# Kernel optimization log

Hardware: AMD Instinct MI355X
Metric: run time of the kernel (lower is better)

## Reference

```python
import jax, jax.numpy as jnp
import numpy as np

B, S, D, H = 4, 2048, 512, 8
DK = D // H


def setup_inputs() -> dict:
    key = jax.random.key(0)
    ks = jax.random.split(key, 11)
    scale = 1.0 / np.sqrt(D)
    inp = {
        'q': jax.random.normal(ks[0], (B, S, D), jnp.float32),
        'k': jax.random.normal(ks[1], (B, S, D), jnp.float32),
        'v': jax.random.normal(ks[2], (B, S, D), jnp.float32),
        'mask': jnp.tril(jnp.ones((S, S), jnp.int32))[None, None, :, :],  # [1,1,S,S] causal
        'w_q': jax.random.normal(ks[3], (D, D), jnp.float32) * scale,
        'b_q': jnp.zeros((D,), jnp.float32),
        'w_k': jax.random.normal(ks[4], (D, D), jnp.float32) * scale,
        'b_k': jnp.zeros((D,), jnp.float32),
        'w_v': jax.random.normal(ks[5], (D, D), jnp.float32) * scale,
        'b_v': jnp.zeros((D,), jnp.float32),
        'w_o': jax.random.normal(ks[6], (D, D), jnp.float32) * scale,
        'b_o': jnp.zeros((D,), jnp.float32),
    }
    return inp


def reference(q, k, v, mask, w_q, b_q, w_k, b_k, w_v, b_v, w_o, b_o):
    # QKV projections (nn.Linear: x @ W^T + b)
    def split_heads(x):  # [B,S,D] -> [B,H,S,DK]
        return x.reshape(B, S, H, DK).transpose(0, 2, 1, 3)

    qh = split_heads(q @ w_q.T + b_q)
    kh = split_heads(k @ w_k.T + b_k)
    vh = split_heads(v @ w_v.T + b_v)

    scores = jnp.einsum('bhqd,bhkd->bhqk', qh, kh) / jnp.sqrt(jnp.float32(DK))
    scores = jnp.where(mask == 0, jnp.float32(-1e9), scores)
    attn = jax.nn.softmax(scores, axis=-1)  # dropout is identity in eval
    ctx = jnp.einsum('bhqk,bhkd->bhqd', attn, vh)  # [B,H,S,DK]
    ctx = ctx.transpose(0, 2, 1, 3).reshape(B, S, D)
    return ctx @ w_o.T + b_o
```

## Files before the change

### kernel.cpp

```cpp
#include <hip/hip_runtime.h>
#include <hip/hip_bf16.h>


#define BATCH  4
#define SLEN   2048
#define DMODEL 512
#define NHEAD  8
#define DHEAD  64
#define MROWS  (BATCH * SLEN)

#define NQ ((size_t)MROWS * DMODEL)
#define NW ((size_t)DMODEL * DMODEL)
#define NB ((size_t)DMODEL)
#define CVT_TOTAL (3 * NQ + 4 * NW + 4 * NB)

#define SCALE_L2E 0.180336880f

typedef short bf16x8 __attribute__((ext_vector_type(8)));
typedef float f32x4  __attribute__((ext_vector_type(4)));

typedef unsigned int __attribute__((address_space(1))) glb_u32_t;
typedef unsigned int __attribute__((address_space(3))) lds_u32_t;

__device__ __forceinline__ void async_copy16(const unsigned short* g, unsigned short* l) {
    __builtin_amdgcn_global_load_lds((glb_u32_t*)g, (lds_u32_t*)l, 16, 0, 0);
}

__device__ __forceinline__ float bf2f(unsigned short u) {
    union { unsigned int i; float f; } v; v.i = ((unsigned int)u) << 16; return v.f;
}
__device__ __forceinline__ unsigned short f2bf(float f) {
    union { float f; unsigned int i; } v; v.f = f;
    unsigned int x = v.i;
    return (unsigned short)((x + 0x7fffu + ((x >> 16) & 1u)) >> 16);
}
__device__ __forceinline__ unsigned int pkbf(float a, float b) {
    union { __hip_bfloat162 h; unsigned int u; } cv;
    cv.h = __float22bfloat162_rn(float2{a, b});
    return cv.u;
}

__device__ __forceinline__ void wait0_barrier() {
    asm volatile("s_waitcnt vmcnt(0)" ::: "memory");
    __builtin_amdgcn_s_barrier();
    asm volatile("" ::: "memory");
}

__global__ __launch_bounds__(256)
void cvt_kernel(const float* __restrict__ q, const float* __restrict__ k,
                const float* __restrict__ v,
                const float* __restrict__ wq, const float* __restrict__ wk,
                const float* __restrict__ wv, const float* __restrict__ wo,
                const float* __restrict__ bq, const float* __restrict__ bk,
                const float* __restrict__ bv, const float* __restrict__ bo,
                unsigned short* __restrict__ dst)
{
    const size_t i4 = ((size_t)blockIdx.x * 256 + threadIdx.x) * 4;
    if (i4 >= CVT_TOTAL) return;
    const float* src;
    size_t off;
    if      (i4 <     NQ)          { src = q;  off = i4; }
    else if (i4 < 2 * NQ)          { src = k;  off = i4 - NQ; }
    else if (i4 < 3 * NQ)          { src = v;  off = i4 - 2 * NQ; }
    else if (i4 < 3 * NQ + NW)     { src = wq; off = i4 - 3 * NQ; }
    else if (i4 < 3 * NQ + 2 * NW) { src = wk; off = i4 - 3 * NQ - NW; }
    else if (i4 < 3 * NQ + 3 * NW) { src = wv; off = i4 - 3 * NQ - 2 * NW; }
    else if (i4 < 3 * NQ + 4 * NW) { src = wo; off = i4 - 3 * NQ - 3 * NW; }
    else if (i4 < 3 * NQ + 4 * NW + NB)     { src = bq; off = i4 - 3 * NQ - 4 * NW; }
    else if (i4 < 3 * NQ + 4 * NW + 2 * NB) { src = bk; off = i4 - 3 * NQ - 4 * NW - NB; }
    else if (i4 < 3 * NQ + 4 * NW + 3 * NB) { src = bv; off = i4 - 3 * NQ - 4 * NW - 2 * NB; }
    else                                    { src = bo; off = i4 - 3 * NQ - 4 * NW - 3 * NB; }
    const float4 f = *(const float4*)(src + off);
    ushort4 o;
    o.x = f2bf(f.x); o.y = f2bf(f.y); o.z = f2bf(f.z); o.w = f2bf(f.w);
    *(ushort4*)(dst + i4) = o;
}

template <typename OutT>
__device__ __forceinline__ void gemm_body(const unsigned short* __restrict__ A,
                                          const unsigned short* __restrict__ W,
                                          const unsigned short* __restrict__ bias,
                                          OutT* __restrict__ C, int mode)
{
    __shared__ __align__(16) unsigned short As[2][128 * 32];
    __shared__ __align__(16) unsigned short Bs[2][128 * 32];

    const int tid  = threadIdx.x;
    const int wave = tid >> 6;
    const int lane = tid & 63;
    const int l15  = lane & 15;
    const int quad = lane >> 4;
    const int m0   = blockIdx.x * 128;
    const int n0   = blockIdx.y * 128;
    const int wm   = (wave & 1) * 64;
    const int wn   = (wave >> 1) * 64;
    const int srow = lane >> 2;
    const int scol = (((lane & 3) ^ (srow & 3)) * 8);
    const int rsw  = (quad ^ (l15 & 3)) * 8;

    auto stage = [&](int k0, int buf) {
        async_copy16(A + (size_t)(m0 + wave * 16 + srow) * DMODEL + k0 + scol, As[buf] + wave * 512);
        async_copy16(A + (size_t)(m0 + (wave + 4) * 16 + srow) * DMODEL + k0 + scol, As[buf] + (wave + 4) * 512);
        async_copy16(W + (size_t)(n0 + wave * 16 + srow) * DMODEL + k0 + scol, Bs[buf] + wave * 512);
        async_copy16(W + (size_t)(n0 + (wave + 4) * 16 + srow) * DMODEL + k0 + scol, Bs[buf] + (wave + 4) * 512);
    };

    f32x4 acc[4][4] = {};
    stage(0, 0);

    #pragma unroll 1
    for (int kt = 0; kt < 16; kt++) {
        const int cur = kt & 1;
        wait0_barrier();
        if (kt < 15) stage((kt + 1) * 32, cur ^ 1);

        bf16x8 af[4], bfr[4];
        #pragma unroll
        for (int i = 0; i < 4; i++)
            af[i] = *(const bf16x8*)(As[cur] + (wm + i * 16 + l15) * 32 + rsw);
        #pragma unroll
        for (int j = 0; j < 4; j++)
            bfr[j] = *(const bf16x8*)(Bs[cur] + (wn + j * 16 + l15) * 32 + rsw);
        #pragma unroll
        for (int i = 0; i < 4; i++)
            #pragma unroll
            for (int j = 0; j < 4; j++)
                acc[i][j] = __builtin_amdgcn_mfma_f32_16x16x32_bf16(af[i], bfr[j], acc[i][j], 0, 0, 0);
    }

    if (mode == 2) {
        #pragma unroll
        for (int j = 0; j < 4; j++) {
            const int col = n0 + wn + j * 16 + l15;
            const float bv = bf2f(bias[col]);
            const int hh = col >> 6, dk = col & 63;
            #pragma unroll
            for (int i = 0; i < 4; i++) {
                const int row = m0 + wm + i * 16 + quad * 4;
                const int bb = row >> 11, s = row & 2047;
                uint2 o2;
                o2.x = pkbf(acc[i][j][0] + bv, acc[i][j][1] + bv);
                o2.y = pkbf(acc[i][j][2] + bv, acc[i][j][3] + bv);
                *(uint2*)((unsigned short*)C + ((size_t)((bb * NHEAD + hh) * DHEAD + dk)) * SLEN + s) = o2;
            }
        }
    } else {
        const float oscale = (mode == 0) ? SCALE_L2E : 1.0f;
        #pragma unroll
        for (int j = 0; j < 4; j++) {
            const int col = n0 + wn + j * 16 + l15;
            const float bv = bf2f(bias[col]);
            #pragma unroll
            for (int i = 0; i < 4; i++) {
                const int row = m0 + wm + i * 16 + quad * 4;
                #pragma unroll
                for (int r = 0; r < 4; r++) {
                    const float val = (acc[i][j][r] + bv) * oscale;
                    if constexpr (sizeof(OutT) == 4)
                        C[(size_t)(row + r) * DMODEL + col] = val;
                    else
                        C[(size_t)(row + r) * DMODEL + col] = f2bf(val);
                }
            }
        }
    }
}

__global__ __launch_bounds__(256, 3)
void qkv_gemm_kernel(const unsigned short* __restrict__ qin,
                     const unsigned short* __restrict__ kin,
                     const unsigned short* __restrict__ vin,
                     const unsigned short* __restrict__ wq,
                     const unsigned short* __restrict__ bq,
                     const unsigned short* __restrict__ wk,
                     const unsigned short* __restrict__ bk,
                     const unsigned short* __restrict__ wv,
                     const unsigned short* __restrict__ bv,
                     unsigned short* __restrict__ qh,
                     unsigned short* __restrict__ kh,
                     unsigned short* __restrict__ vt)
{
    const int z = blockIdx.z;
    const unsigned short* A    = (z == 0) ? qin : (z == 1) ? kin : vin;
    const unsigned short* W    = (z == 0) ? wq  : (z == 1) ? wk  : wv;
    const unsigned short* bias = (z == 0) ? bq  : (z == 1) ? bk  : bv;
    unsigned short*       C    = (z == 0) ? qh  : (z == 1) ? kh  : vt;
    gemm_body<unsigned short>(A, W, bias, C, z);
}

__global__ __launch_bounds__(256, 3)
void oproj_gemm_kernel(const unsigned short* __restrict__ ctx,
                       const unsigned short* __restrict__ wo,
                       const unsigned short* __restrict__ bo,
                       float* __restrict__ out)
{
    gemm_body<float>(ctx, wo, bo, out, 3);
}

__global__ __launch_bounds__(256, 4)
void attn_kernel(const unsigned short* __restrict__ qh,
                 const unsigned short* __restrict__ kh,
                 const unsigned short* __restrict__ vt,
                 unsigned short* __restrict__ ctx)
{
    __shared__ __align__(16) unsigned short Ks[2][64 * 64];
    __shared__ __align__(16) unsigned short Vs[2][64 * 64];
    __shared__ __align__(16) unsigned short Ps[4 * 16 * 64];

    const int tid  = threadIdx.x;
    const int wave = tid >> 6;
    const int lane = tid & 63;
    const int l15  = lane & 15;
    const int quad = lane >> 4;

    const int bh = blockIdx.x;
    const int x  = blockIdx.y;
    const int g  = x & 7, s = x >> 3;
    const int qt = (s == 0) ? g : (s == 1) ? 15 - g : (s == 2) ? 16 + g : 31 - g;
    const int b  = bh >> 3;
    const int h  = bh & 7;

    const size_t base = (size_t)b * SLEN * DMODEL + (size_t)h * DHEAD;
    const unsigned short* Q  = qh + base;
    const unsigned short* K  = kh + base;
    const unsigned short* VT = vt + (size_t)bh * DHEAD * SLEN;

    const int krow_l = lane >> 3;
    const int kcol_l = ((lane & 7) ^ (krow_l & 7)) * 8;

    const int qrow = qt * 64 + wave * 16 + l15;
    bf16x8 qf0 = *(const bf16x8*)(Q + (size_t)qrow * DMODEL + quad * 8);
    bf16x8 qf1 = *(const bf16x8*)(Q + (size_t)qrow * DMODEL + 32 + quad * 8);

    f32x4 oacc[4] = {};
    float lsum = 0.0f;

    unsigned short* Pw = Ps + wave * (16 * 64);
    const int ktiles = qt + 1;

    auto stageKV = [&](int kt, int buf) {
        async_copy16(K + (size_t)(kt * 64 + wave * 8 + krow_l) * DMODEL + kcol_l,
                     Ks[buf] + wave * 512);
        async_copy16(K + (size_t)(kt * 64 + (wave + 4) * 8 + krow_l) * DMODEL + kcol_l,
                     Ks[buf] + (wave + 4) * 512);
        async_copy16(VT + (size_t)(wave * 8 + krow_l) * SLEN + kt * 64 + kcol_l,
                     Vs[buf] + wave * 512);
        async_copy16(VT + (size_t)((wave + 4) * 8 + krow_l) * SLEN + kt * 64 + kcol_l,
                     Vs[buf] + (wave + 4) * 512);
    };

    stageKV(0, 0);

    #pragma unroll 1
    for (int kt = 0; kt < ktiles; kt++) {
        const int cur = kt & 1;
        wait0_barrier();
        if (kt + 1 < ktiles) stageKV(kt + 1, cur ^ 1);

        f32x4 sacc[4] = {};
        #pragma unroll
        for (int kk = 0; kk < 2; kk++) {
            const bf16x8 qf = kk ? qf1 : qf0;
            #pragma unroll
            for (int j = 0; j < 4; j++) {
                bf16x8 kf = *(const bf16x8*)(Ks[cur] + (j * 16 + l15) * 64
                                                + (((kk * 4 + quad) ^ (l15 & 7)) * 8));
                sacc[j] = __builtin_amdgcn_mfma_f32_16x16x32_bf16(kf, qf, sacc[j], 0, 0, 0);
            }
        }

        if (kt == qt) {
            #pragma unroll
            for (int j = 0; j < 4; j++)
                #pragma unroll
                for (int r = 0; r < 4; r++) {
                    const int kv = kt * 64 + j * 16 + quad * 4 + r;
                    if (kv > qrow) sacc[j][r] = -1e30f;
                }
        }

        #pragma unroll
        for (int j = 0; j < 4; j++) {
            const float p0 = exp2f(sacc[j][0]);
            const float p1 = exp2f(sacc[j][1]);
            const float p2v = exp2f(sacc[j][2]);
            const float p3 = exp2f(sacc[j][3]);
            lsum += (p0 + p1) + (p2v + p3);
            uint2 pw;
            pw.x = pkbf(p0, p1);
            pw.y = pkbf(p2v, p3);
            const int chunk = (j * 2 + (quad >> 1)) ^ (l15 & 7);
            *(uint2*)(Pw + l15 * 64 + chunk * 8 + (quad & 1) * 4) = pw;
        }
        asm volatile("s_waitcnt lgkmcnt(0)" ::: "memory");

        #pragma unroll
        for (int kk = 0; kk < 2; kk++) {
            bf16x8 pf = *(const bf16x8*)(Pw + l15 * 64 + (((kk * 4 + quad) ^ (l15 & 7)) * 8));
            #pragma unroll
            for (int jd = 0; jd < 4; jd++) {
                bf16x8 vf = *(const bf16x8*)(Vs[cur] + (jd * 16 + l15) * 64
                                                + (((kk * 4 + quad) ^ (l15 & 7)) * 8));
                oacc[jd] = __builtin_amdgcn_mfma_f32_16x16x32_bf16(vf, pf, oacc[jd], 0, 0, 0);
            }
        }
    }

    lsum += __shfl_xor(lsum, 16, 64);
    lsum += __shfl_xor(lsum, 32, 64);
    const float invl = 1.0f / lsum;

    #pragma unroll
    for (int jd = 0; jd < 4; jd++) {
        uint2 o2;
        o2.x = pkbf(oacc[jd][0] * invl, oacc[jd][1] * invl);
        o2.y = pkbf(oacc[jd][2] * invl, oacc[jd][3] * invl);
        *(uint2*)(ctx + base + (size_t)qrow * DMODEL + jd * 16 + quad * 4) = o2;
    }
}

extern "C" void kernel_launch(void* const* d_in, const int* in_sizes, int n_in,
                              void* d_out, int out_size, void* d_ws, size_t ws_size,
                              hipStream_t stream)
{
    const float* q   = (const float*)d_in[0];
    const float* k   = (const float*)d_in[1];
    const float* v   = (const float*)d_in[2];
    const float* w_q = (const float*)d_in[4];
    const float* b_q = (const float*)d_in[5];
    const float* w_k = (const float*)d_in[6];
    const float* b_k = (const float*)d_in[7];
    const float* w_v = (const float*)d_in[8];
    const float* b_v = (const float*)d_in[9];
    const float* w_o = (const float*)d_in[10];
    const float* b_o = (const float*)d_in[11];
    float* out = (float*)d_out;

    unsigned short* ws = (unsigned short*)d_ws;
    unsigned short* qb  = ws;
    unsigned short* kb  = ws + NQ;
    unsigned short* vb  = ws + 2 * NQ;
    unsigned short* wqb = ws + 3 * NQ;
    unsigned short* wkb = wqb + NW;
    unsigned short* wvb = wkb + NW;
    unsigned short* wob = wvb + NW;
    unsigned short* bqb = wob + NW;
    unsigned short* bkb = bqb + NB;
    unsigned short* bvb = bkb + NB;
    unsigned short* bob = bvb + NB;
    unsigned short* qh  = bob + NB;
    unsigned short* kh  = qh + NQ;
    unsigned short* vt  = kh + NQ;
    unsigned short* ctx = vt + NQ;

    dim3 blk(256);
    hipLaunchKernelGGL(cvt_kernel, dim3((unsigned)(CVT_TOTAL / 4 / 256)), blk, 0, stream,
                       q, k, v, w_q, w_k, w_v, w_o, b_q, b_k, b_v, b_o, ws);
    hipLaunchKernelGGL(qkv_gemm_kernel, dim3(MROWS / 128, DMODEL / 128, 3), blk, 0, stream,
                       qb, kb, vb, wqb, bqb, wkb, bkb, wvb, bvb, qh, kh, vt);
    hipLaunchKernelGGL(attn_kernel, dim3(BATCH * NHEAD, 32), blk, 0, stream,
                       qh, kh, vt, ctx);
    hipLaunchKernelGGL(oproj_gemm_kernel, dim3(MROWS / 128, DMODEL / 128), blk, 0, stream,
                       ctx, wob, bob, out);
}
```

Before: 198.1 us.

## Pair complementary causal query tiles per block to share K/V staging

Each attention block now processes two query tiles, g and 31-g, in a single pass over key tiles. For the first g+1 key tiles both tiles' scores and PV products come from the same staged K/V in LDS, so K/V loads and barriers for those tiles are shared. Every block also gets the same total amount of causal work, which balances the load. The grid is halved, the P scratch buffer doubled and launch bounds relaxed to 2 to allow more registers, at the cost of fewer resident waves to hide latency.

New measurement: 198.7 us. Within noise of the previous version (+0.3%).

```diff
diff --git a/kernel.cpp b/kernel.cpp
--- a/kernel.cpp
+++ b/kernel.cpp
@@ -197,7 +197,7 @@
     gemm_body<float>(ctx, wo, bo, out, 3);
 }
 
-__global__ __launch_bounds__(256, 4)
+__global__ __launch_bounds__(256, 2)
 void attn_kernel(const unsigned short* __restrict__ qh,
                  const unsigned short* __restrict__ kh,
                  const unsigned short* __restrict__ vt,
@@ -205,7 +205,7 @@
 {
     __shared__ __align__(16) unsigned short Ks[2][64 * 64];
     __shared__ __align__(16) unsigned short Vs[2][64 * 64];
-    __shared__ __align__(16) unsigned short Ps[4 * 16 * 64];
+    __shared__ __align__(16) unsigned short Ps[4 * 2 * 16 * 64];
 
     const int tid  = threadIdx.x;
     const int wave = tid >> 6;
@@ -215,8 +215,9 @@
 
     const int bh = blockIdx.x;
     const int x  = blockIdx.y;
-    const int g  = x & 7, s = x >> 3;
-    const int qt = (s == 0) ? g : (s == 1) ? 15 - g : (s == 2) ? 16 + g : 31 - g;
+    const int g  = (x < 8) ? x : 23 - x;
+    const int qta = g;
+    const int qtb = 31 - g;
     const int b  = bh >> 3;
     const int h  = bh & 7;
 
@@ -228,15 +229,19 @@
     const int krow_l = lane >> 3;
     const int kcol_l = ((lane & 7) ^ (krow_l & 7)) * 8;
 
-    const int qrow = qt * 64 + wave * 16 + l15;
-    bf16x8 qf0 = *(const bf16x8*)(Q + (size_t)qrow * DMODEL + quad * 8);
-    bf16x8 qf1 = *(const bf16x8*)(Q + (size_t)qrow * DMODEL + 32 + quad * 8);
-
-    f32x4 oacc[4] = {};
-    float lsum = 0.0f;
-
-    unsigned short* Pw = Ps + wave * (16 * 64);
-    const int ktiles = qt + 1;
+    const int qrow_a = qta * 64 + wave * 16 + l15;
+    const int qrow_b = qtb * 64 + wave * 16 + l15;
+    const bf16x8 qa0 = *(const bf16x8*)(Q + (size_t)qrow_a * DMODEL + quad * 8);
+    const bf16x8 qa1 = *(const bf16x8*)(Q + (size_t)qrow_a * DMODEL + 32 + quad * 8);
+    const bf16x8 qb0 = *(const bf16x8*)(Q + (size_t)qrow_b * DMODEL + quad * 8);
+    const bf16x8 qb1 = *(const bf16x8*)(Q + (size_t)qrow_b * DMODEL + 32 + quad * 8);
+
+    f32x4 oacc_a[4] = {};
+    f32x4 oacc_b[4] = {};
+    float lsum_a = 0.0f, lsum_b = 0.0f;
+
+    unsigned short* Pa = Ps + (wave * 2 + 0) * (16 * 64);
+    unsigned short* Pb = Ps + (wave * 2 + 1) * (16 * 64);
 
     auto stageKV = [&](int kt, int buf) {
         async_copy16(K + (size_t)(kt * 64 + wave * 8 + krow_l) * DMODEL + kcol_l,
@@ -249,36 +254,7 @@
                      Vs[buf] + (wave + 4) * 512);
     };
 
-    stageKV(0, 0);
-
-    #pragma unroll 1
-    for (int kt = 0; kt < ktiles; kt++) {
-        const int cur = kt & 1;
-        wait0_barrier();
-        if (kt + 1 < ktiles) stageKV(kt + 1, cur ^ 1);
-
-        f32x4 sacc[4] = {};
-        #pragma unroll
-        for (int kk = 0; kk < 2; kk++) {
-            const bf16x8 qf = kk ? qf1 : qf0;
-            #pragma unroll
-            for (int j = 0; j < 4; j++) {
-                bf16x8 kf = *(const bf16x8*)(Ks[cur] + (j * 16 + l15) * 64
-                                                + (((kk * 4 + quad) ^ (l15 & 7)) * 8));
-                sacc[j] = __builtin_amdgcn_mfma_f32_16x16x32_bf16(kf, qf, sacc[j], 0, 0, 0);
-            }
-        }
-
-        if (kt == qt) {
-            #pragma unroll
-            for (int j = 0; j < 4; j++)
-                #pragma unroll
-                for (int r = 0; r < 4; r++) {
-                    const int kv = kt * 64 + j * 16 + quad * 4 + r;
-                    if (kv > qrow) sacc[j][r] = -1e30f;
-                }
-        }
-
+    auto softmax_pack = [&](f32x4* sacc, unsigned short* Pw, float& lsum) {
         #pragma unroll
         for (int j = 0; j < 4; j++) {
             const float p0 = exp2f(sacc[j][0]);
@@ -292,30 +268,112 @@
             const int chunk = (j * 2 + (quad >> 1)) ^ (l15 & 7);
             *(uint2*)(Pw + l15 * 64 + chunk * 8 + (quad & 1) * 4) = pw;
         }
-        asm volatile("s_waitcnt lgkmcnt(0)" ::: "memory");
-
-        #pragma unroll
-        for (int kk = 0; kk < 2; kk++) {
-            bf16x8 pf = *(const bf16x8*)(Pw + l15 * 64 + (((kk * 4 + quad) ^ (l15 & 7)) * 8));
-            #pragma unroll
-            for (int jd = 0; jd < 4; jd++) {
-                bf16x8 vf = *(const bf16x8*)(Vs[cur] + (jd * 16 + l15) * 64
-                                                + (((kk * 4 + quad) ^ (l15 & 7)) * 8));
-                oacc[jd] = __builtin_amdgcn_mfma_f32_16x16x32_bf16(vf, pf, oacc[jd], 0, 0, 0);
+    };
+
+    auto diag_mask = [&](f32x4* sacc, int kt, int qrow) {
+        #pragma unroll
+        for (int j = 0; j < 4; j++)
+            #pragma unroll
+            for (int r = 0; r < 4; r++) {
+                const int kv = kt * 64 + j * 16 + quad * 4 + r;
+                if (kv > qrow) sacc[j][r] = -1e30f;
+            }
+    };
+
+    const int nkt = 32 - g;
+    stageKV(0, 0);
+
+    #pragma unroll 1
+    for (int kt = 0; kt < nkt; kt++) {
+        const int cur = kt & 1;
+        wait0_barrier();
+        if (kt + 1 < nkt) stageKV(kt + 1, cur ^ 1);
+
+        if (kt <= g) {
+            f32x4 sa[4] = {}, sb[4] = {};
+            #pragma unroll
+            for (int kk = 0; kk < 2; kk++) {
+                const bf16x8 qfa = kk ? qa1 : qa0;
+                const bf16x8 qfb = kk ? qb1 : qb0;
+                #pragma unroll
+                for (int j = 0; j < 4; j++) {
+                    bf16x8 kf = *(const bf16x8*)(Ks[cur] + (j * 16 + l15) * 64
+                                                    + (((kk * 4 + quad) ^ (l15 & 7)) * 8));
+                    sb[j] = __builtin_amdgcn_mfma_f32_16x16x32_bf16(kf, qfb, sb[j], 0, 0, 0);
+                    sa[j] = __builtin_amdgcn_mfma_f32_16x16x32_bf16(kf, qfa, sa[j], 0, 0, 0);
+                }
+            }
+            if (kt == qta) diag_mask(sa, kt, qrow_a);
+            softmax_pack(sa, Pa, lsum_a);
+            softmax_pack(sb, Pb, lsum_b);
+            asm volatile("s_waitcnt lgkmcnt(0)" ::: "memory");
+
+            #pragma unroll
+            for (int kk = 0; kk < 2; kk++) {
+                bf16x8 pfa = *(const bf16x8*)(Pa + l15 * 64 + (((kk * 4 + quad) ^ (l15 & 7)) * 8));
+                bf16x8 pfb = *(const bf16x8*)(Pb + l15 * 64 + (((kk * 4 + quad) ^ (l15 & 7)) * 8));
+                #pragma unroll
+                for (int jd = 0; jd < 4; jd++) {
+                    bf16x8 vf = *(const bf16x8*)(Vs[cur] + (jd * 16 + l15) * 64
+                                                    + (((kk * 4 + quad) ^ (l15 & 7)) * 8));
+                    oacc_a[jd] = __builtin_amdgcn_mfma_f32_16x16x32_bf16(vf, pfa, oacc_a[jd], 0, 0, 0);
+                    oacc_b[jd] = __builtin_amdgcn_mfma_f32_16x16x32_bf16(vf, pfb, oacc_b[jd], 0, 0, 0);
+                }
+            }
+        } else {
+            f32x4 sb[4] = {};
+            #pragma unroll
+            for (int kk = 0; kk < 2; kk++) {
+                const bf16x8 qfb = kk ? qb1 : qb0;
+                #pragma unroll
+                for (int j = 0; j < 4; j++) {
+                    bf16x8 kf = *(const bf16x8*)(Ks[cur] + (j * 16 + l15) * 64
+                                                    + (((kk * 4 + quad) ^ (l15 & 7)) * 8));
+                    sb[j] = __builtin_amdgcn_mfma_f32_16x16x32_bf16(kf, qfb, sb[j], 0, 0, 0);
+                }
+            }
+            if (kt == qtb) diag_mask(sb, kt, qrow_b);
+            softmax_pack(sb, Pb, lsum_b);
+            asm volatile("s_waitcnt lgkmcnt(0)" ::: "memory");
+
+            #pragma unroll
+            for (int kk = 0; kk < 2; kk++) {
+                bf16x8 pfb = *(const bf16x8*)(Pb + l15 * 64 + (((kk * 4 + quad) ^ (l15 & 7)) * 8));
+                #pragma unroll
+                for (int jd = 0; jd < 4; jd++) {
+                    bf16x8 vf = *(const bf16x8*)(Vs[cur] + (jd * 16 + l15) * 64
+                                                    + (((kk * 4 + quad) ^ (l15 & 7)) * 8));
+                    oacc_b[jd] = __builtin_amdgcn_mfma_f32_16x16x32_bf16(vf, pfb, oacc_b[jd], 0, 0, 0);
+                }
             }
         }
     }
 
-    lsum += __shfl_xor(lsum, 16, 64);
-    lsum += __shfl_xor(lsum, 32, 64);
-    const float invl = 1.0f / lsum;
-
-    #pragma unroll
-    for (int jd = 0; jd < 4; jd++) {
-        uint2 o2;
-        o2.x = pkbf(oacc[jd][0] * invl, oacc[jd][1] * invl);
-        o2.y = pkbf(oacc[jd][2] * invl, oacc[jd][3] * invl);
-        *(uint2*)(ctx + base + (size_t)qrow * DMODEL + jd * 16 + quad * 4) = o2;
+    {
+        float la = lsum_a;
+        la += __shfl_xor(la, 16, 64);
+        la += __shfl_xor(la, 32, 64);
+        const float invla = 1.0f / la;
+        #pragma unroll
+        for (int jd = 0; jd < 4; jd++) {
+            uint2 o2;
+            o2.x = pkbf(oacc_a[jd][0] * invla, oacc_a[jd][1] * invla);
+            o2.y = pkbf(oacc_a[jd][2] * invla, oacc_a[jd][3] * invla);
+            *(uint2*)(ctx + base + (size_t)qrow_a * DMODEL + jd * 16 + quad * 4) = o2;
+        }
+    }
+    {
+        float lb = lsum_b;
+        lb += __shfl_xor(lb, 16, 64);
+        lb += __shfl_xor(lb, 32, 64);
+        const float invlb = 1.0f / lb;
+        #pragma unroll
+        for (int jd = 0; jd < 4; jd++) {
+            uint2 o2;
+            o2.x = pkbf(oacc_b[jd][0] * invlb, oacc_b[jd][1] * invlb);
+            o2.y = pkbf(oacc_b[jd][2] * invlb, oacc_b[jd][3] * invlb);
+            *(uint2*)(ctx + base + (size_t)qrow_b * DMODEL + jd * 16 + quad * 4) = o2;
+        }
     }
 }
 
@@ -358,7 +416,7 @@
                        q, k, v, w_q, w_k, w_v, w_o, b_q, b_k, b_v, b_o, ws);
     hipLaunchKernelGGL(qkv_gemm_kernel, dim3(MROWS / 128, DMODEL / 128, 3), blk, 0, stream,
                        qb, kb, vb, wqb, bqb, wkb, bkb, wvb, bvb, qh, kh, vt);
-    hipLaunchKernelGGL(attn_kernel, dim3(BATCH * NHEAD, 32), blk, 0, stream,
+    hipLaunchKernelGGL(attn_kernel, dim3(BATCH * NHEAD, 16), blk, 0, stream,
                        qh, kh, vt, ctx);
     hipLaunchKernelGGL(oproj_gemm_kernel, dim3(MROWS / 128, DMODEL / 128), blk, 0, stream,
                        ctx, wob, bob, out);
```

## Fuse pipeline into one cooperative persistent kernel with grid barriers

Applied to the files above, without the earlier changes.

Replaces the four launches with a single cooperative kernel of 768 blocks that converts the weights, runs the QKV projection, attention and output projection, and separates the stages with global atomic barriers. The QKV GEMM now loads the fp32 activations directly into LDS and converts them to bf16 in registers, so the separate pass that wrote bf16 copies of q, k and v is gone. Attention tiles are paired long with short to balance causal work across blocks, and the output projection moves to 64x64 tiles so the grid is covered. The intent is to cut launch overhead and the activation conversion traffic. In exchange it adds spin-barrier costs, a memset, and a fallback multi-kernel path if the cooperative launch fails.

New measurement: 696.3 us. +251.5%, slower.

```diff
diff --git a/kernel.cpp b/kernel.cpp
--- a/kernel.cpp
+++ b/kernel.cpp
@@ -12,7 +12,9 @@
 #define NQ ((size_t)MROWS * DMODEL)
 #define NW ((size_t)DMODEL * DMODEL)
 #define NB ((size_t)DMODEL)
-#define CVT_TOTAL (3 * NQ + 4 * NW + 4 * NB)
+#define CVTW_TOTAL (4 * NW + 4 * NB)
+
+#define GRID_P 768
 
 #define SCALE_L2E 0.180336880f
 
@@ -22,7 +24,7 @@
 typedef unsigned int __attribute__((address_space(1))) glb_u32_t;
 typedef unsigned int __attribute__((address_space(3))) lds_u32_t;
 
-__device__ __forceinline__ void async_copy16(const unsigned short* g, unsigned short* l) {
+__device__ __forceinline__ void async16(const void* g, void* l) {
     __builtin_amdgcn_global_load_lds((glb_u32_t*)g, (lds_u32_t*)l, 16, 0, 0);
 }
 
@@ -46,81 +48,80 @@
     asm volatile("" ::: "memory");
 }
 
-__global__ __launch_bounds__(256)
-void cvt_kernel(const float* __restrict__ q, const float* __restrict__ k,
-                const float* __restrict__ v,
-                const float* __restrict__ wq, const float* __restrict__ wk,
-                const float* __restrict__ wv, const float* __restrict__ wo,
-                const float* __restrict__ bq, const float* __restrict__ bk,
-                const float* __restrict__ bv, const float* __restrict__ bo,
-                unsigned short* __restrict__ dst)
-{
-    const size_t i4 = ((size_t)blockIdx.x * 256 + threadIdx.x) * 4;
-    if (i4 >= CVT_TOTAL) return;
-    const float* src;
-    size_t off;
-    if      (i4 <     NQ)          { src = q;  off = i4; }
-    else if (i4 < 2 * NQ)          { src = k;  off = i4 - NQ; }
-    else if (i4 < 3 * NQ)          { src = v;  off = i4 - 2 * NQ; }
-    else if (i4 < 3 * NQ + NW)     { src = wq; off = i4 - 3 * NQ; }
-    else if (i4 < 3 * NQ + 2 * NW) { src = wk; off = i4 - 3 * NQ - NW; }
-    else if (i4 < 3 * NQ + 3 * NW) { src = wv; off = i4 - 3 * NQ - 2 * NW; }
-    else if (i4 < 3 * NQ + 4 * NW) { src = wo; off = i4 - 3 * NQ - 3 * NW; }
-    else if (i4 < 3 * NQ + 4 * NW + NB)     { src = bq; off = i4 - 3 * NQ - 4 * NW; }
-    else if (i4 < 3 * NQ + 4 * NW + 2 * NB) { src = bk; off = i4 - 3 * NQ - 4 * NW - NB; }
-    else if (i4 < 3 * NQ + 4 * NW + 3 * NB) { src = bv; off = i4 - 3 * NQ - 4 * NW - 2 * NB; }
-    else                                    { src = bo; off = i4 - 3 * NQ - 4 * NW - 3 * NB; }
-    const float4 f = *(const float4*)(src + off);
-    ushort4 o;
-    o.x = f2bf(f.x); o.y = f2bf(f.y); o.z = f2bf(f.z); o.w = f2bf(f.w);
-    *(ushort4*)(dst + i4) = o;
-}
-
-template <typename OutT>
-__device__ __forceinline__ void gemm_body(const unsigned short* __restrict__ A,
-                                          const unsigned short* __restrict__ W,
-                                          const unsigned short* __restrict__ bias,
-                                          OutT* __restrict__ C, int mode)
-{
-    __shared__ __align__(16) unsigned short As[2][128 * 32];
-    __shared__ __align__(16) unsigned short Bs[2][128 * 32];
+__device__ __forceinline__ void gbar(unsigned* c) {
+    __syncthreads();
+    if (threadIdx.x == 0) {
+        __threadfence();
+        __hip_atomic_fetch_add(c, 1u, __ATOMIC_RELEASE, __HIP_MEMORY_SCOPE_AGENT);
+        while (__hip_atomic_load(c, __ATOMIC_ACQUIRE, __HIP_MEMORY_SCOPE_AGENT) < gridDim.x)
+            __builtin_amdgcn_s_sleep(8);
+    }
+    __syncthreads();
+}
+
+__device__ __forceinline__ void qkv_body(const float* __restrict__ A,
+                                         const unsigned short* __restrict__ W,
+                                         const unsigned short* __restrict__ bias,
+                                         unsigned short* __restrict__ C,
+                                         int mode, int m0, int n0,
+                                         unsigned char* smem)
+{
+    float*          Asf = (float*)smem;
+    unsigned short* Bs  = (unsigned short*)(smem + 32768);
 
     const int tid  = threadIdx.x;
     const int wave = tid >> 6;
     const int lane = tid & 63;
     const int l15  = lane & 15;
     const int quad = lane >> 4;
-    const int m0   = blockIdx.x * 128;
-    const int n0   = blockIdx.y * 128;
     const int wm   = (wave & 1) * 64;
     const int wn   = (wave >> 1) * 64;
     const int srow = lane >> 2;
     const int scol = (((lane & 3) ^ (srow & 3)) * 8);
-    const int rsw  = (quad ^ (l15 & 3)) * 8;
-
-    auto stage = [&](int k0, int buf) {
-        async_copy16(A + (size_t)(m0 + wave * 16 + srow) * DMODEL + k0 + scol, As[buf] + wave * 512);
-        async_copy16(A + (size_t)(m0 + (wave + 4) * 16 + srow) * DMODEL + k0 + scol, As[buf] + (wave + 4) * 512);
-        async_copy16(W + (size_t)(n0 + wave * 16 + srow) * DMODEL + k0 + scol, Bs[buf] + wave * 512);
-        async_copy16(W + (size_t)(n0 + (wave + 4) * 16 + srow) * DMODEL + k0 + scol, Bs[buf] + (wave + 4) * 512);
+    const int rswb = (quad ^ (l15 & 3)) * 8;
+    const int krow = lane >> 3;
+    const int acol = ((lane & 7) ^ (krow & 7)) * 4;
+
+    auto stageA = [&](int k0, int buf) {
+        #pragma unroll
+        for (int c = 0; c < 4; c++) {
+            const int rb = c * 32 + wave * 8;
+            async16(A + (size_t)(m0 + rb + krow) * DMODEL + k0 + acol,
+                    Asf + (size_t)buf * 4096 + rb * 32);
+        }
     };
+    auto stageW = [&](int k0, int buf) {
+        async16(W + (size_t)(n0 + wave * 16 + srow) * DMODEL + k0 + scol,
+                Bs + (size_t)buf * 4096 + wave * 512);
+        async16(W + (size_t)(n0 + (wave + 4) * 16 + srow) * DMODEL + k0 + scol,
+                Bs + (size_t)buf * 4096 + (wave + 4) * 512);
+    };
 
     f32x4 acc[4][4] = {};
-    stage(0, 0);
+    stageA(0, 0);
+    stageW(0, 0);
 
     #pragma unroll 1
     for (int kt = 0; kt < 16; kt++) {
         const int cur = kt & 1;
         wait0_barrier();
-        if (kt < 15) stage((kt + 1) * 32, cur ^ 1);
+        if (kt < 15) { stageA((kt + 1) * 32, cur ^ 1); stageW((kt + 1) * 32, cur ^ 1); }
 
         bf16x8 af[4], bfr[4];
         #pragma unroll
-        for (int i = 0; i < 4; i++)
-            af[i] = *(const bf16x8*)(As[cur] + (wm + i * 16 + l15) * 32 + rsw);
+        for (int i = 0; i < 4; i++) {
+            const int row = wm + i * 16 + l15;
+            const float* rp = Asf + (size_t)cur * 4096 + row * 32;
+            const f32x4 x = *(const f32x4*)(rp + (((quad * 2)     ^ (row & 7)) * 4));
+            const f32x4 y = *(const f32x4*)(rp + (((quad * 2 + 1) ^ (row & 7)) * 4));
+            union { bf16x8 v; unsigned int u[4]; } r;
+            r.u[0] = pkbf(x[0], x[1]); r.u[1] = pkbf(x[2], x[3]);
+            r.u[2] = pkbf(y[0], y[1]); r.u[3] = pkbf(y[2], y[3]);
+            af[i] = r.v;
+        }
         #pragma unroll
         for (int j = 0; j < 4; j++)
-            bfr[j] = *(const bf16x8*)(Bs[cur] + (wn + j * 16 + l15) * 32 + rsw);
+            bfr[j] = *(const bf16x8*)(Bs + (size_t)cur * 4096 + (wn + j * 16 + l15) * 32 + rswb);
         #pragma unroll
         for (int i = 0; i < 4; i++)
             #pragma unroll
@@ -141,7 +142,7 @@
                 uint2 o2;
                 o2.x = pkbf(acc[i][j][0] + bv, acc[i][j][1] + bv);
                 o2.y = pkbf(acc[i][j][2] + bv, acc[i][j][3] + bv);
-                *(uint2*)((unsigned short*)C + ((size_t)((bb * NHEAD + hh) * DHEAD + dk)) * SLEN + s) = o2;
+                *(uint2*)(C + ((size_t)((bb * NHEAD + hh) * DHEAD + dk)) * SLEN + s) = o2;
             }
         }
     } else {
@@ -154,71 +155,29 @@
             for (int i = 0; i < 4; i++) {
                 const int row = m0 + wm + i * 16 + quad * 4;
                 #pragma unroll
-                for (int r = 0; r < 4; r++) {
-                    const float val = (acc[i][j][r] + bv) * oscale;
-                    if constexpr (sizeof(OutT) == 4)
-                        C[(size_t)(row + r) * DMODEL + col] = val;
-                    else
-                        C[(size_t)(row + r) * DMODEL + col] = f2bf(val);
-                }
+                for (int r = 0; r < 4; r++)
+                    C[(size_t)(row + r) * DMODEL + col] = f2bf((acc[i][j][r] + bv) * oscale);
             }
         }
     }
 }
 
-__global__ __launch_bounds__(256, 3)
-void qkv_gemm_kernel(const unsigned short* __restrict__ qin,
-                     const unsigned short* __restrict__ kin,
-                     const unsigned short* __restrict__ vin,
-                     const unsigned short* __restrict__ wq,
-                     const unsigned short* __restrict__ bq,
-                     const unsigned short* __restrict__ wk,
-                     const unsigned short* __restrict__ bk,
-                     const unsigned short* __restrict__ wv,
-                     const unsigned short* __restrict__ bv,
-                     unsigned short* __restrict__ qh,
-                     unsigned short* __restrict__ kh,
-                     unsigned short* __restrict__ vt)
-{
-    const int z = blockIdx.z;
-    const unsigned short* A    = (z == 0) ? qin : (z == 1) ? kin : vin;
-    const unsigned short* W    = (z == 0) ? wq  : (z == 1) ? wk  : wv;
-    const unsigned short* bias = (z == 0) ? bq  : (z == 1) ? bk  : bv;
-    unsigned short*       C    = (z == 0) ? qh  : (z == 1) ? kh  : vt;
-    gemm_body<unsigned short>(A, W, bias, C, z);
-}
-
-__global__ __launch_bounds__(256, 3)
-void oproj_gemm_kernel(const unsigned short* __restrict__ ctx,
-                       const unsigned short* __restrict__ wo,
-                       const unsigned short* __restrict__ bo,
-                       float* __restrict__ out)
-{
-    gemm_body<float>(ctx, wo, bo, out, 3);
-}
-
-__global__ __launch_bounds__(256, 4)
-void attn_kernel(const unsigned short* __restrict__ qh,
-                 const unsigned short* __restrict__ kh,
-                 const unsigned short* __restrict__ vt,
-                 unsigned short* __restrict__ ctx)
-{
-    __shared__ __align__(16) unsigned short Ks[2][64 * 64];
-    __shared__ __align__(16) unsigned short Vs[2][64 * 64];
-    __shared__ __align__(16) unsigned short Ps[4 * 16 * 64];
+__device__ __forceinline__ void attn_body(const unsigned short* __restrict__ qh,
+                                          const unsigned short* __restrict__ kh,
+                                          const unsigned short* __restrict__ vt,
+                                          unsigned short* __restrict__ ctx,
+                                          int bh, int qt, unsigned char* smem)
+{
+    unsigned short* Ks = (unsigned short*)smem;
+    unsigned short* Vs = Ks + 2 * 64 * 64;
+    unsigned short* Ps = Vs + 2 * 64 * 64;
 
     const int tid  = threadIdx.x;
     const int wave = tid >> 6;
     const int lane = tid & 63;
     const int l15  = lane & 15;
     const int quad = lane >> 4;
-
-    const int bh = blockIdx.x;
-    const int x  = blockIdx.y;
-    const int g  = x & 7, s = x >> 3;
-    const int qt = (s == 0) ? g : (s == 1) ? 15 - g : (s == 2) ? 16 + g : 31 - g;
-    const int b  = bh >> 3;
-    const int h  = bh & 7;
+    const int b = bh >> 3, h = bh & 7;
 
     const size_t base = (size_t)b * SLEN * DMODEL + (size_t)h * DHEAD;
     const unsigned short* Q  = qh + base;
@@ -229,24 +188,23 @@
     const int kcol_l = ((lane & 7) ^ (krow_l & 7)) * 8;
 
     const int qrow = qt * 64 + wave * 16 + l15;
-    bf16x8 qf0 = *(const bf16x8*)(Q + (size_t)qrow * DMODEL + quad * 8);
-    bf16x8 qf1 = *(const bf16x8*)(Q + (size_t)qrow * DMODEL + 32 + quad * 8);
+    const bf16x8 qf0 = *(const bf16x8*)(Q + (size_t)qrow * DMODEL + quad * 8);
+    const bf16x8 qf1 = *(const bf16x8*)(Q + (size_t)qrow * DMODEL + 32 + quad * 8);
 
     f32x4 oacc[4] = {};
     float lsum = 0.0f;
-
     unsigned short* Pw = Ps + wave * (16 * 64);
     const int ktiles = qt + 1;
 
     auto stageKV = [&](int kt, int buf) {
-        async_copy16(K + (size_t)(kt * 64 + wave * 8 + krow_l) * DMODEL + kcol_l,
-                     Ks[buf] + wave * 512);
-        async_copy16(K + (size_t)(kt * 64 + (wave + 4) * 8 + krow_l) * DMODEL + kcol_l,
-                     Ks[buf] + (wave + 4) * 512);
-        async_copy16(VT + (size_t)(wave * 8 + krow_l) * SLEN + kt * 64 + kcol_l,
-                     Vs[buf] + wave * 512);
-        async_copy16(VT + (size_t)((wave + 4) * 8 + krow_l) * SLEN + kt * 64 + kcol_l,
-                     Vs[buf] + (wave + 4) * 512);
+        async16(K + (size_t)(kt * 64 + wave * 8 + krow_l) * DMODEL + kcol_l,
+                Ks + (size_t)buf * 4096 + wave * 512);
+        async16(K + (size_t)(kt * 64 + (wave + 4) * 8 + krow_l) * DMODEL + kcol_l,
+                Ks + (size_t)buf * 4096 + (wave + 4) * 512);
+        async16(VT + (size_t)(wave * 8 + krow_l) * SLEN + kt * 64 + kcol_l,
+                Vs + (size_t)buf * 4096 + wave * 512);
+        async16(VT + (size_t)((wave + 4) * 8 + krow_l) * SLEN + kt * 64 + kcol_l,
+                Vs + (size_t)buf * 4096 + (wave + 4) * 512);
     };
 
     stageKV(0, 0);
@@ -263,7 +221,7 @@
             const bf16x8 qf = kk ? qf1 : qf0;
             #pragma unroll
             for (int j = 0; j < 4; j++) {
-                bf16x8 kf = *(const bf16x8*)(Ks[cur] + (j * 16 + l15) * 64
+                bf16x8 kf = *(const bf16x8*)(Ks + (size_t)cur * 4096 + (j * 16 + l15) * 64
                                                 + (((kk * 4 + quad) ^ (l15 & 7)) * 8));
                 sacc[j] = __builtin_amdgcn_mfma_f32_16x16x32_bf16(kf, qf, sacc[j], 0, 0, 0);
             }
@@ -299,7 +257,7 @@
             bf16x8 pf = *(const bf16x8*)(Pw + l15 * 64 + (((kk * 4 + quad) ^ (l15 & 7)) * 8));
             #pragma unroll
             for (int jd = 0; jd < 4; jd++) {
-                bf16x8 vf = *(const bf16x8*)(Vs[cur] + (jd * 16 + l15) * 64
+                bf16x8 vf = *(const bf16x8*)(Vs + (size_t)cur * 4096 + (jd * 16 + l15) * 64
                                                 + (((kk * 4 + quad) ^ (l15 & 7)) * 8));
                 oacc[jd] = __builtin_amdgcn_mfma_f32_16x16x32_bf16(vf, pf, oacc[jd], 0, 0, 0);
             }
@@ -317,6 +275,213 @@
         o2.y = pkbf(oacc[jd][2] * invl, oacc[jd][3] * invl);
         *(uint2*)(ctx + base + (size_t)qrow * DMODEL + jd * 16 + quad * 4) = o2;
     }
+}
+
+__device__ __forceinline__ void oproj_body(const unsigned short* __restrict__ ctx,
+                                           const unsigned short* __restrict__ wo,
+                                           const unsigned short* __restrict__ bo,
+                                           float* __restrict__ out,
+                                           int m0, int n0, unsigned char* smem)
+{
+    unsigned short* As = (unsigned short*)smem;
+    unsigned short* Bs = As + 2 * 64 * 32;
+
+    const int tid  = threadIdx.x;
+    const int wave = tid >> 6;
+    const int lane = tid & 63;
+    const int l15  = lane & 15;
+    const int quad = lane >> 4;
+    const int wm   = (wave & 1) * 32;
+    const int wn   = (wave >> 1) * 32;
+    const int srow = lane >> 2;
+    const int scol = (((lane & 3) ^ (srow & 3)) * 8);
+    const int rsw  = (quad ^ (l15 & 3)) * 8;
+
+    auto stage = [&](int k0, int buf) {
+        async16(ctx + (size_t)(m0 + wave * 16 + srow) * DMODEL + k0 + scol,
+                As + (size_t)buf * 2048 + wave * 512);
+        async16(wo + (size_t)(n0 + wave * 16 + srow) * DMODEL + k0 + scol,
+                Bs + (size_t)buf * 2048 + wave * 512);
+    };
+
+    f32x4 acc[2][2] = {};
+    stage(0, 0);
+
+    #pragma unroll 1
+    for (int kt = 0; kt < 16; kt++) {
+        const int cur = kt & 1;
+        wait0_barrier();
+        if (kt < 15) stage((kt + 1) * 32, cur ^ 1);
+
+        bf16x8 af[2], bfr[2];
+        #pragma unroll
+        for (int i = 0; i < 2; i++)
+            af[i] = *(const bf16x8*)(As + (size_t)cur * 2048 + (wm + i * 16 + l15) * 32 + rsw);
+        #pragma unroll
+        for (int j = 0; j < 2; j++)
+            bfr[j] = *(const bf16x8*)(Bs + (size_t)cur * 2048 + (wn + j * 16 + l15) * 32 + rsw);
+        #pragma unroll
+        for (int i = 0; i < 2; i++)
+            #pragma unroll
+            for (int j = 0; j < 2; j++)
+                acc[i][j] = __builtin_amdgcn_mfma_f32_16x16x32_bf16(af[i], bfr[j], acc[i][j], 0, 0, 0);
+    }
+
+    #pragma unroll
+    for (int j = 0; j < 2; j++) {
+        const int col = n0 + wn + j * 16 + l15;
+        const float bv = bf2f(bo[col]);
+        #pragma unroll
+        for (int i = 0; i < 2; i++) {
+            const int row = m0 + wm + i * 16 + quad * 4;
+            #pragma unroll
+            for (int r = 0; r < 4; r++)
+                out[(size_t)(row + r) * DMODEL + col] = acc[i][j][r] + bv;
+        }
+    }
+}
+
+__global__ __launch_bounds__(256, 3)
+void fused_kernel(const float* __restrict__ q, const float* __restrict__ k,
+                  const float* __restrict__ v,
+                  const float* __restrict__ wqf, const float* __restrict__ bqf,
+                  const float* __restrict__ wkf, const float* __restrict__ bkf,
+                  const float* __restrict__ wvf, const float* __restrict__ bvf,
+                  const float* __restrict__ wof, const float* __restrict__ bof,
+                  float* __restrict__ out, unsigned short* __restrict__ ws)
+{
+    __shared__ __align__(16) unsigned char smem[49152];
+
+    unsigned* ctr = (unsigned*)ws;
+    unsigned short* wqb = ws + 3 * NQ;
+    unsigned short* wkb = wqb + NW;
+    unsigned short* wvb = wkb + NW;
+    unsigned short* wob = wvb + NW;
+    unsigned short* bqb = wob + NW;
+    unsigned short* bkb = bqb + NB;
+    unsigned short* bvb = bkb + NB;
+    unsigned short* bob = bvb + NB;
+    unsigned short* qh  = bob + NB;
+    unsigned short* kh  = qh + NQ;
+    unsigned short* vt  = kh + NQ;
+    unsigned short* ctx = vt + NQ;
+
+    const int id = blockIdx.x;
+
+    for (size_t i4 = ((size_t)id * 256 + threadIdx.x) * 4; i4 < CVTW_TOTAL;
+         i4 += (size_t)gridDim.x * 256 * 4) {
+        const float* src; size_t off;
+        if      (i4 <     NW)          { src = wqf; off = i4; }
+        else if (i4 < 2 * NW)          { src = wkf; off = i4 - NW; }
+        else if (i4 < 3 * NW)          { src = wvf; off = i4 - 2 * NW; }
+        else if (i4 < 4 * NW)          { src = wof; off = i4 - 3 * NW; }
+        else if (i4 < 4 * NW + NB)     { src = bqf; off = i4 - 4 * NW; }
+        else if (i4 < 4 * NW + 2 * NB) { src = bkf; off = i4 - 4 * NW - NB; }
+        else if (i4 < 4 * NW + 3 * NB) { src = bvf; off = i4 - 4 * NW - 2 * NB; }
+        else                           { src = bof; off = i4 - 4 * NW - 3 * NB; }
+        const float4 f = *(const float4*)(src + off);
+        ushort4 o;
+        o.x = f2bf(f.x); o.y = f2bf(f.y); o.z = f2bf(f.z); o.w = f2bf(f.w);
+        *(ushort4*)(wqb + i4) = o;
+    }
+    gbar(ctr + 0);
+
+    {
+        const int x = id & 63, y = (id >> 6) & 3, z = id >> 8;
+        const float*          Az = (z == 0) ? q   : (z == 1) ? k   : v;
+        const unsigned short* Wz = (z == 0) ? wqb : (z == 1) ? wkb : wvb;
+        const unsigned short* Bz = (z == 0) ? bqb : (z == 1) ? bkb : bvb;
+        unsigned short*       Cz = (z == 0) ? qh  : (z == 1) ? kh  : vt;
+        qkv_body(Az, Wz, Bz, Cz, z, x * 128, y * 128, smem);
+    }
+    gbar(ctr + 1);
+
+    {
+        const int a = id >> 5, bh = id & 31;
+        const int qt0 = (a < 8) ? 31 - a : (a < 16) ? 23 - a : a - 16;
+        attn_body(qh, kh, vt, ctx, bh, qt0, smem);
+        if (id < 256) {
+            __syncthreads();
+            attn_body(qh, kh, vt, ctx, bh, 16 + a, smem);
+        }
+    }
+    gbar(ctr + 2);
+
+    {
+        oproj_body(ctx, wob, bob, out, (id >> 3) * 64, (id & 7) * 64, smem);
+        if (id < 256) {
+            __syncthreads();
+            const int j = id + 768;
+            oproj_body(ctx, wob, bob, out, (j >> 3) * 64, (j & 7) * 64, smem);
+        }
+    }
+}
+
+__global__ __launch_bounds__(256)
+void cvt_w_kernel(const float* __restrict__ wq, const float* __restrict__ wk,
+                  const float* __restrict__ wv, const float* __restrict__ wo,
+                  const float* __restrict__ bq, const float* __restrict__ bk,
+                  const float* __restrict__ bv, const float* __restrict__ bo,
+                  unsigned short* __restrict__ dst)
+{
+    const size_t i4 = ((size_t)blockIdx.x * 256 + threadIdx.x) * 4;
+    if (i4 >= CVTW_TOTAL) return;
+    const float* src;
+    size_t off;
+    if      (i4 <     NW)          { src = wq; off = i4; }
+    else if (i4 < 2 * NW)          { src = wk; off = i4 - NW; }
+    else if (i4 < 3 * NW)          { src = wv; off = i4 - 2 * NW; }
+    else if (i4 < 4 * NW)          { src = wo; off = i4 - 3 * NW; }
+    else if (i4 < 4 * NW + NB)     { src = bq; off = i4 - 4 * NW; }
+    else if (i4 < 4 * NW + 2 * NB) { src = bk; off = i4 - 4 * NW - NB; }
+    else if (i4 < 4 * NW + 3 * NB) { src = bv; off = i4 - 4 * NW - 2 * NB; }
+    else                           { src = bo; off = i4 - 4 * NW - 3 * NB; }
+    const float4 f = *(const float4*)(src + off);
+    ushort4 o;
+    o.x = f2bf(f.x); o.y = f2bf(f.y); o.z = f2bf(f.z); o.w = f2bf(f.w);
+    *(ushort4*)(dst + i4) = o;
+}
+
+__global__ __launch_bounds__(256, 3)
+void qkv_gemm_kernel(const float* __restrict__ qin, const float* __restrict__ kin,
+                     const float* __restrict__ vin,
+                     const unsigned short* __restrict__ wq, const unsigned short* __restrict__ bq,
+                     const unsigned short* __restrict__ wk, const unsigned short* __restrict__ bk,
+                     const unsigned short* __restrict__ wv, const unsigned short* __restrict__ bv,
+                     unsigned short* __restrict__ qh, unsigned short* __restrict__ kh,
+                     unsigned short* __restrict__ vt)
+{
+    __shared__ __align__(16) unsigned char smem[49152];
+    const int z = blockIdx.z;
+    const float*          A    = (z == 0) ? qin : (z == 1) ? kin : vin;
+    const unsigned short* W    = (z == 0) ? wq  : (z == 1) ? wk  : wv;
+    const unsigned short* bias = (z == 0) ? bq  : (z == 1) ? bk  : bv;
+    unsigned short*       C    = (z == 0) ? qh  : (z == 1) ? kh  : vt;
+    qkv_body(A, W, bias, C, z, blockIdx.x * 128, blockIdx.y * 128, smem);
+}
+
+__global__ __launch_bounds__(256, 4)
+void attn_kernel(const unsigned short* __restrict__ qh,
+                 const unsigned short* __restrict__ kh,
+                 const unsigned short* __restrict__ vt,
+                 unsigned short* __restrict__ ctx)
+{
+    __shared__ __align__(16) unsigned char smem[40960];
+    const int bh = blockIdx.x;
+    const int x  = blockIdx.y;
+    const int g  = x & 7, s = x >> 3;
+    const int qt = (s == 0) ? g : (s == 1) ? 15 - g : (s == 2) ? 16 + g : 31 - g;
+    attn_body(qh, kh, vt, ctx, bh, qt, smem);
+}
+
+__global__ __launch_bounds__(256, 4)
+void oproj_gemm_kernel(const unsigned short* __restrict__ ctx,
+                       const unsigned short* __restrict__ wo,
+                       const unsigned short* __restrict__ bo,
+                       float* __restrict__ out)
+{
+    __shared__ __align__(16) unsigned char smem[16384];
+    oproj_body(ctx, wo, bo, out, blockIdx.x * 64, blockIdx.y * 64, smem);
 }
 
 extern "C" void kernel_launch(void* const* d_in, const int* in_sizes, int n_in,
@@ -335,31 +500,41 @@
     const float* w_o = (const float*)d_in[10];
     const float* b_o = (const float*)d_in[11];
     float* out = (float*)d_out;
-
     unsigned short* ws = (unsigned short*)d_ws;
-    unsigned short* qb  = ws;
-    unsigned short* kb  = ws + NQ;
-    unsigned short* vb  = ws + 2 * NQ;
-    unsigned short* wqb = ws + 3 * NQ;
-    unsigned short* wkb = wqb + NW;
-    unsigned short* wvb = wkb + NW;
-    unsigned short* wob = wvb + NW;
-    unsigned short* bqb = wob + NW;
-    unsigned short* bkb = bqb + NB;
-    unsigned short* bvb = bkb + NB;
-    unsigned short* bob = bvb + NB;
-    unsigned short* qh  = bob + NB;
-    unsigned short* kh  = qh + NQ;
-    unsigned short* vt  = kh + NQ;
-    unsigned short* ctx = vt + NQ;
-
-    dim3 blk(256);
-    hipLaunchKernelGGL(cvt_kernel, dim3((unsigned)(CVT_TOTAL / 4 / 256)), blk, 0, stream,
-                       q, k, v, w_q, w_k, w_v, w_o, b_q, b_k, b_v, b_o, ws);
-    hipLaunchKernelGGL(qkv_gemm_kernel, dim3(MROWS / 128, DMODEL / 128, 3), blk, 0, stream,
-                       qb, kb, vb, wqb, bqb, wkb, bkb, wvb, bvb, qh, kh, vt);
-    hipLaunchKernelGGL(attn_kernel, dim3(BATCH * NHEAD, 32), blk, 0, stream,
-                       qh, kh, vt, ctx);
-    hipLaunchKernelGGL(oproj_gemm_kernel, dim3(MROWS / 128, DMODEL / 128), blk, 0, stream,
-                       ctx, wob, bob, out);
-}
+
+    hipMemsetAsync(ws, 0, 128, stream);
+
+    void* args[] = {
+        (void*)&q, (void*)&k, (void*)&v,
+        (void*)&w_q, (void*)&b_q, (void*)&w_k, (void*)&b_k,
+        (void*)&w_v, (void*)&b_v, (void*)&w_o, (void*)&b_o,
+        (void*)&out, (void*)&ws
+    };
+    hipError_t rc = hipLaunchCooperativeKernel((const void*)fused_kernel,
+                                               dim3(GRID_P), dim3(256),
+                                               args, 0, stream);
+    if (rc != hipSuccess) {
+        unsigned short* wqb = ws + 3 * NQ;
+        unsigned short* wkb = wqb + NW;
+        unsigned short* wvb = wkb + NW;
+        unsigned short* wob = wvb + NW;
+        unsigned short* bqb = wob + NW;
+        unsigned short* bkb = bqb + NB;
+        unsigned short* bvb = bkb + NB;
+        unsigned short* bob = bvb + NB;
+        unsigned short* qh  = bob + NB;
+        unsigned short* kh  = qh + NQ;
+        unsigned short* vt  = kh + NQ;
+        unsigned short* ctx = vt + NQ;
+
+        dim3 blk(256);
+        hipLaunchKernelGGL(cvt_w_kernel, dim3((unsigned)(CVTW_TOTAL / 4 / 256)), blk, 0, stream,
+                           w_q, w_k, w_v, w_o, b_q, b_k, b_v, b_o, wqb);
+        hipLaunchKernelGGL(qkv_gemm_kernel, dim3(MROWS / 128, DMODEL / 128, 3), blk, 0, stream,
+                           q, k, v, wqb, bqb, wkb, bkb, wvb, bvb, qh, kh, vt);
+        hipLaunchKernelGGL(attn_kernel, dim3(BATCH * NHEAD, 32), blk, 0, stream,
+                           qh, kh, vt, ctx);
+        hipLaunchKernelGGL(oproj_gemm_kernel, dim3(MROWS / 64, DMODEL / 64), blk, 0, stream,
+                           ctx, wob, bob, out);
+    }
+}
```
